# Performance work log

Hardware: AMD Instinct MI355X
Metric: run time of the kernel (lower is better)

The kernel has to match this reference:

```python
import jax, jax.numpy as jnp
import numpy as np

EPS = 1e-6

def rmsnorm(x, w):
    # RMSNorm over last dim (head_dim), eps=1e-6, learned scale w
    return x * jax.lax.rsqrt(jnp.mean(x * x, axis=-1, keepdims=True) + EPS) * w

def setup_inputs() -> dict:
    key = jax.random.key(0)
    ks = jax.random.split(key, 8)
    B, L, D = 2, 256, 4096          # batch, new-chunk len, model dim
    H, Dh = 32, 128                  # heads, head_dim (H*Dh == D)
    SINK, LOCAL = 128, 4096          # attention-sink + sliding window
    S = SINK + LOCAL                 # fixed cache length
    s = 0.02
    return {
        "x": jax.random.normal(ks[0], (B, L, D), jnp.float32),
        "cache_k": jax.random.normal(ks[1], (B, S, H, Dh), jnp.float32),
        "cache_v": jax.random.normal(ks[2], (B, S, H, Dh), jnp.float32),
        "Wq": jax.random.normal(ks[3], (D, H * Dh), jnp.float32) * s,
        "Wk": jax.random.normal(ks[4], (D, H * Dh), jnp.float32) * s,
        "Wv": jax.random.normal(ks[5], (D, H * Dh), jnp.float32) * s,
        "Wo": jax.random.normal(ks[6], (H * Dh, D), jnp.float32) * s,
        "q_norm_w": jnp.ones((Dh,), jnp.float32),
        "k_norm_w": jnp.ones((Dh,), jnp.float32),
        "sink": 128,
    }

def reference(x, cache_k, cache_v, Wq, Wk, Wv, Wo, q_norm_w, k_norm_w, sink):
    B, L, D = x.shape
    S, H, Dh = cache_k.shape[1], cache_k.shape[2], cache_k.shape[3]
    # QKV projections (bias=False) + per-head RMSNorm on q and k
    q = rmsnorm((x @ Wq).reshape(B, L, H, Dh), q_norm_w)
    k = rmsnorm((x @ Wk).reshape(B, L, H, Dh), k_norm_w)
    v = (x @ Wv).reshape(B, L, H, Dh)
    # steady-state cache: keep sink tokens, roll local window left by L, write new chunk at tail
    new_k = jnp.concatenate([cache_k[:, :sink], cache_k[:, sink + L:], k], axis=1)  # [B,S,H,Dh]
    new_v = jnp.concatenate([cache_v[:, :sink], cache_v[:, sink + L:], v], axis=1)
    scale = 1.0 / jnp.sqrt(jnp.asarray(Dh, x.dtype))
    logits = jnp.einsum('blhd,bshd->bhls', q, new_k) * scale  # [B,H,L,S]
    # causal within the new chunk: query i sees cache positions j <= (S-L)+i
    i = jnp.arange(L)[:, None]
    j = jnp.arange(S)[None, :]
    mask = j <= (S - L) + i
    logits = jnp.where(mask[None, None], logits, jnp.finfo(logits.dtype).min)
    attn = jax.nn.softmax(logits, axis=-1)
    out = jnp.einsum('bhls,bshd->blhd', attn, new_v).reshape(B, L, H * Dh)
    return out @ Wo
```

## Files before the change

kernel.cpp:

```cpp
#include <hip/hip_runtime.h>
#include <stdint.h>
#include <stddef.h>

typedef unsigned short u16;
typedef __bf16 bf16x8 __attribute__((ext_vector_type(8)));
typedef float f32x4 __attribute__((ext_vector_type(4)));
typedef u16 u16x8 __attribute__((ext_vector_type(8)));

#define B_    2
#define L_    256
#define D_    4096
#define H_    32
#define DH_   128
#define SINK_ 128
#define S_    4224
#define WINS_ 3968
#define M_    512
#define SPLIT_ 4

__device__ __forceinline__ float bf2f(u16 u){
  union { float f; uint32_t i; } v; v.i = ((uint32_t)u) << 16; return v.f;
}
__device__ __forceinline__ u16 f2bf(float f){
  union { float f; uint32_t i; } v; v.f = f;
  return (u16)((v.i + 0x7fffu + ((v.i >> 16) & 1u)) >> 16);
}
__device__ __forceinline__ bf16x8 ld8(const u16* p){
  return __builtin_bit_cast(bf16x8, *(const u16x8*)p);
}
__device__ __forceinline__ bf16x8 ld8f(const float* p){
  f32x4 a = *(const f32x4*)p;
  f32x4 b = *(const f32x4*)(p + 4);
  u16x8 r;
  r[0] = f2bf(a[0]); r[1] = f2bf(a[1]); r[2] = f2bf(a[2]); r[3] = f2bf(a[3]);
  r[4] = f2bf(b[0]); r[5] = f2bf(b[1]); r[6] = f2bf(b[2]); r[7] = f2bf(b[3]);
  return __builtin_bit_cast(bf16x8, r);
}

__global__ void detect_k(const u16* __restrict__ x, uint32_t* __restrict__ flag){
  const int lane = threadIdx.x & 63;
  int bad = 0;
  for (int i = lane; i < 1024; i += 64){
    float v = bf2f(x[2 * i]);
    if (!(v * 0.0f == 0.0f) || fabsf(v) > 1e6f) bad = 1;
  }
#pragma unroll
  for (int m = 1; m < 64; m <<= 1) bad |= __shfl_xor(bad, m, 64);
  if (threadIdx.x == 0) *flag = (uint32_t)(bad ? 1 : 0);
}

__global__ __launch_bounds__(256) void transpose_k(const void* __restrict__ W,
                                                   u16* __restrict__ WT,
                                                   const uint32_t* __restrict__ flag){
  const int mode = (int)*flag;
  __shared__ u16 Ts[64 * 68];
  const int t  = threadIdx.x;
  const int k0 = blockIdx.x * 64;
  const int n0 = blockIdx.y * 64;
  const int r  = t >> 2;
  const int c  = (t & 3) * 8;
  const size_t rowoff = (size_t)(k0 + r) * 4096;
#pragma unroll
  for (int p = 0; p < 2; p++){
    const int cc = c + p * 32;
    u16x8 v;
    if (mode){
      const float* pf = (const float*)W + rowoff + n0 + cc;
      f32x4 a = *(const f32x4*)pf;
      f32x4 b = *(const f32x4*)(pf + 4);
      v[0] = f2bf(a[0]); v[1] = f2bf(a[1]); v[2] = f2bf(a[2]); v[3] = f2bf(a[3]);
      v[4] = f2bf(b[0]); v[5] = f2bf(b[1]); v[6] = f2bf(b[2]); v[7] = f2bf(b[3]);
    } else {
      v = *(const u16x8*)((const u16*)W + rowoff + n0 + cc);
    }
#pragma unroll
    for (int j = 0; j < 8; j++) Ts[r * 68 + cc + j] = v[j];
  }
  __syncthreads();
#pragma unroll
  for (int p = 0; p < 2; p++){
    const int kc = c + p * 32;
    u16x8 v;
#pragma unroll
    for (int j = 0; j < 8; j++) v[j] = Ts[(kc + j) * 68 + r];
    *(u16x8*)(WT + (size_t)(n0 + r) * 4096 + k0 + kc) = v;
  }
}

__global__ __launch_bounds__(256) void gemm64_k(const void* __restrict__ Ain,
                                                const u16* __restrict__ BT3,
                                                void* __restrict__ Cout,
                                                const uint32_t* __restrict__ flag,
                                                int a_ext, int c_ext){
  const int mode = (int)*flag;
  const int a_f32 = a_ext & mode;
  const int c_f32 = c_ext & mode;

  const int bx = blockIdx.x;
  const int wi = bx >> 6;
  const int n0 = (bx & 63) * 64;
  const int m0 = blockIdx.y * 64;
  const u16* BT = BT3 + (size_t)wi * (4096ull * 4096);

  __shared__ u16 As[64 * 32];
  __shared__ u16 Bs[64 * 32];

  const int t    = threadIdx.x;
  const int w    = t >> 6;
  const int lane = t & 63;
  const int wm   = w >> 1;
  const int wn   = w & 1;
  const int mq   = lane & 15;
  const int qd   = lane >> 4;

  f32x4 acc[2][2] = {};

  const size_t ga = (size_t)(m0 + (t >> 2)) * 4096 + (t & 3) * 8;
  const size_t gb = (size_t)(n0 + (t >> 2)) * 4096 + (t & 3) * 8;

  for (int kt = 0; kt < 128; kt++){
    const int k0 = kt * 32;
    u16x8 av;
    if (a_f32){
      const float* pa = (const float*)Ain + ga + k0;
      f32x4 a = *(const f32x4*)pa;
      f32x4 b = *(const f32x4*)(pa + 4);
      av[0] = f2bf(a[0]); av[1] = f2bf(a[1]); av[2] = f2bf(a[2]); av[3] = f2bf(a[3]);
      av[4] = f2bf(b[0]); av[5] = f2bf(b[1]); av[6] = f2bf(b[2]); av[7] = f2bf(b[3]);
    } else {
      av = *(const u16x8*)((const u16*)Ain + ga + k0);
    }
    u16x8 bv = *(const u16x8*)(BT + gb + k0);
    __syncthreads();
    *(u16x8*)&As[t * 8] = av;
    *(u16x8*)&Bs[t * 8] = bv;
    __syncthreads();

    bf16x8 af[2], bfr[2];
#pragma unroll
    for (int i = 0; i < 2; i++)
      af[i] = ld8(&As[(wm * 32 + i * 16 + mq) * 32 + qd * 8]);
#pragma unroll
    for (int j = 0; j < 2; j++)
      bfr[j] = ld8(&Bs[(wn * 32 + j * 16 + mq) * 32 + qd * 8]);
#pragma unroll
    for (int i = 0; i < 2; i++)
#pragma unroll
      for (int j = 0; j < 2; j++)
        acc[i][j] = __builtin_amdgcn_mfma_f32_16x16x32_bf16(af[i], bfr[j], acc[i][j], 0, 0, 0);
  }

  u16* cu = (u16*)Cout + (size_t)wi * ((size_t)M_ * 4096);
#pragma unroll
  for (int i = 0; i < 2; i++)
#pragma unroll
    for (int j = 0; j < 2; j++)
#pragma unroll
      for (int r = 0; r < 4; r++){
        const int row = m0 + wm * 32 + i * 16 + qd * 4 + r;
        const int col = n0 + wn * 32 + j * 16 + mq;
        if (c_f32) ((float*)Cout)[(size_t)row * 4096 + col] = acc[i][j][r];
        else       cu[(size_t)row * 4096 + col]             = f2bf(acc[i][j][r]);
      }
}

__global__ __launch_bounds__(256) void rmsnorm_k(const u16* __restrict__ src,
                                                 u16* __restrict__ dst,
                                                 const void* __restrict__ wq,
                                                 const void* __restrict__ wk,
                                                 const uint32_t* __restrict__ flag){
  const int mode = (int)*flag;
  const int t = threadIdx.x, w = t >> 6, lane = t & 63;
  const size_t base = (size_t)blockIdx.y * (size_t)M_ * 4096;
  const int rid = blockIdx.x * 4 + w;
  const u16* s = src + base + (size_t)rid * 128 + lane * 2;
  u16*       d = dst + base + (size_t)rid * 128 + lane * 2;
  const void* wp = blockIdx.y ? wk : wq;
  float w0, w1;
  if (mode){ w0 = ((const float*)wp)[lane * 2]; w1 = ((const float*)wp)[lane * 2 + 1]; }
  else     { w0 = bf2f(((const u16*)wp)[lane * 2]); w1 = bf2f(((const u16*)wp)[lane * 2 + 1]); }
  const float f0 = bf2f(s[0]), f1 = bf2f(s[1]);
  float ss = f0 * f0 + f1 * f1;
#pragma unroll
  for (int m = 1; m < 64; m <<= 1) ss += __shfl_xor(ss, m, 64);
  const float rinv = rsqrtf(ss * (1.0f / 128.0f) + 1e-6f);
  d[0] = f2bf(f0 * rinv * w0);
  d[1] = f2bf(f1 * rinv * w1);
}

__global__ __launch_bounds__(512, 4) void attn_k(const u16* __restrict__ qn,
                                                 const u16* __restrict__ kn,
                                                 const u16* __restrict__ vnew,
                                                 const void* __restrict__ ck,
                                                 const void* __restrict__ cv,
                                                 u16* __restrict__ ao,
                                                 const uint32_t* __restrict__ flag){
  const int mode = (int)*flag;
  __shared__ __align__(16) unsigned char LDSB[51200];
  u16*   VTall = (u16*)LDSB;
  u16*   PBall = (u16*)(LDSB + 40960);
  float* OB    = (float*)LDSB;
  float* ML    = (float*)(LDSB + 16384);

  const int t  = threadIdx.x;
  const int W  = t >> 6;
  const int sp = W >> 1;
  const int w  = W & 1;
  const int lane = t & 63;
  const int lt = t & 127;
  const int blk = blockIdx.x;
  const int b  = blk >> 8;
  const int h  = (blk >> 3) & 31;
  const int qt = blk & 7;
  const int q0 = qt * 32 + w * 16;
  const int mq = lane & 15;
  const int qd = lane >> 4;

  u16* VT = VTall + sp * (128 * 40);
  u16* pb = PBall + W * 640;

  bf16x8 aq[4];
  {
    const u16* qp = qn + ((size_t)(b * L_ + q0 + mq)) * 4096 + h * 128 + qd * 8;
#pragma unroll
    for (int kc = 0; kc < 4; kc++) aq[kc] = ld8(qp + kc * 32);
  }

  f32x4 oacc[8] = {};
  float mi[4], li[4];
#pragma unroll
  for (int r = 0; r < 4; r++){ mi[r] = -1e30f; li[r] = 0.f; }

  const int nchunks = (WINS_ + qt * 32 + 63) / 32;
  const int cpb = (nchunks + SPLIT_ - 1) / SPLIT_;
  const int sc_beg = sp * cpb;
  const int sc_end = (sc_beg + cpb < nchunks) ? (sc_beg + cpb) : nchunks;
  const float scale = 0.08838834764831845f;
  const float L2E = 1.4426950408889634f;

  const int dd = lt;
  u16x8 vv[4];

  auto loadV = [&](int sc){
    const int s0c = sc * 32;
#pragma unroll
    for (int c = 0; c < 4; c++){
#pragma unroll
      for (int j = 0; j < 8; j++){
        const int s = s0c + c * 8 + j;
        u16 val;
        if (s >= WINS_){
          val = vnew[((size_t)(b * L_ + (s - WINS_)) << 12) + h * 128 + dd];
        } else {
          const int scc = (s < SINK_) ? s : (s + L_);
          const size_t off = ((((size_t)b * S_ + scc) * H_ + h) << 7) + dd;
          val = mode ? f2bf(((const float*)cv)[off]) : ((const u16*)cv)[off];
        }
        vv[c][j] = val;
      }
    }
  };

  if (sc_beg < sc_end) loadV(sc_beg);

  for (int scr = 0; scr < cpb; scr++){
    const int sc = sc_beg + scr;
    const int act = (sc < sc_end);
    const int s0 = sc * 32;

    __syncthreads();
    if (act){
#pragma unroll
      for (int c = 0; c < 4; c++)
        *(u16x8*)&VT[dd * 40 + c * 8] = vv[c];
    }
    __syncthreads();
    if (sc + 1 < sc_end) loadV(sc + 1);

    if (act){
      float lg[2][4];
#pragma unroll
      for (int st = 0; st < 2; st++){
        const int s = s0 + st * 16 + mq;
        f32x4 a = {};
        if (s0 + st * 16 >= WINS_){
          const u16* kp = kn + ((size_t)(b * L_ + (s - WINS_)) << 12) + h * 128;
#pragma unroll
          for (int kc = 0; kc < 4; kc++)
            a = __builtin_amdgcn_mfma_f32_16x16x32_bf16(aq[kc], ld8(kp + kc * 32 + qd * 8), a, 0, 0, 0);
        } else if (mode){
          const int scc = (s < SINK_) ? s : (s + L_);
          const float* kp = (const float*)ck + ((((size_t)b * S_ + scc) * H_ + h) << 7);
#pragma unroll
          for (int kc = 0; kc < 4; kc++)
            a = __builtin_amdgcn_mfma_f32_16x16x32_bf16(aq[kc], ld8f(kp + kc * 32 + qd * 8), a, 0, 0, 0);
        } else {
          const int scc = (s < SINK_) ? s : (s + L_);
          const u16* kp = (const u16*)ck + ((((size_t)b * S_ + scc) * H_ + h) << 7);
#pragma unroll
          for (int kc = 0; kc < 4; kc++)
            a = __builtin_amdgcn_mfma_f32_16x16x32_bf16(aq[kc], ld8(kp + kc * 32 + qd * 8), a, 0, 0, 0);
        }
#pragma unroll
        for (int r = 0; r < 4; r++) lg[st][r] = a[r] * scale;
      }
      if (s0 + 31 > WINS_ + q0){
#pragma unroll
        for (int st = 0; st < 2; st++){
          const int s = s0 + st * 16 + mq;
#pragma unroll
          for (int r = 0; r < 4; r++)
            if (s > WINS_ + (q0 + qd * 4 + r)) lg[st][r] = -1e30f;
        }
      }
      float p[2][4];
#pragma unroll
      for (int r = 0; r < 4; r++){
        float mx = fmaxf(lg[0][r], lg[1][r]);
#pragma unroll
        for (int m = 1; m < 16; m <<= 1) mx = fmaxf(mx, __shfl_xor(mx, m, 64));
        const float mnew = fmaxf(mi[r], mx);
        const float alpha = exp2f((mi[r] - mnew) * L2E);
        mi[r] = mnew;
        float s_ = 0.f;
#pragma unroll
        for (int st = 0; st < 2; st++){
          p[st][r] = exp2f((lg[st][r] - mnew) * L2E);
          s_ += p[st][r];
        }
#pragma unroll
        for (int m = 1; m < 16; m <<= 1) s_ += __shfl_xor(s_, m, 64);
        li[r] = li[r] * alpha + s_;
#pragma unroll
        for (int nt = 0; nt < 8; nt++) oacc[nt][r] *= alpha;
      }
#pragma unroll
      for (int st = 0; st < 2; st++)
#pragma unroll
        for (int r = 0; r < 4; r++)
          pb[(qd * 4 + r) * 40 + st * 16 + mq] = f2bf(p[st][r]);
      asm volatile("" ::: "memory");
      u16x8 pr;
#pragma unroll
      for (int j = 0; j < 8; j++) pr[j] = pb[mq * 40 + qd * 8 + j];
      bf16x8 ap = __builtin_bit_cast(bf16x8, pr);
#pragma unroll
      for (int nt = 0; nt < 8; nt++){
        bf16x8 bv = ld8(&VT[(nt * 16 + mq) * 40 + qd * 8]);
        oacc[nt] = __builtin_amdgcn_mfma_f32_16x16x32_bf16(ap, bv, oacc[nt], 0, 0, 0);
      }
    }
  }

  __syncthreads();
  if (mq == 0){
#pragma unroll
    for (int r = 0; r < 4; r++){
      const int lr = w * 16 + qd * 4 + r;
      ML[(sp * 32 + lr) * 2 + 0] = mi[r];
      ML[(sp * 32 + lr) * 2 + 1] = li[r];
    }
  }
  __syncthreads();

  float gl[4], wgt[4];
#pragma unroll
  for (int r = 0; r < 4; r++){
    const int lr = w * 16 + qd * 4 + r;
    float m_ = -1e30f;
#pragma unroll
    for (int p = 0; p < SPLIT_; p++) m_ = fmaxf(m_, ML[(p * 32 + lr) * 2 + 0]);
    float l_ = 0.f;
#pragma unroll
    for (int p = 0; p < SPLIT_; p++)
      l_ += exp2f((ML[(p * 32 + lr) * 2 + 0] - m_) * L2E) * ML[(p * 32 + lr) * 2 + 1];
    gl[r] = l_;
    wgt[r] = exp2f((mi[r] - m_) * L2E);
  }

#pragma unroll
  for (int p = 0; p < SPLIT_; p++){
    if (sp == p){
#pragma unroll
      for (int nt = 0; nt < 8; nt++)
#pragma unroll
        for (int r = 0; r < 4; r++){
          const int off = (w * 16 + qd * 4 + r) * 128 + nt * 16 + mq;
          const float v = wgt[r] * oacc[nt][r];
          if (p == 0) OB[off] = v;
          else        OB[off] += v;
        }
    }
    __syncthreads();
  }

  if (sp == 0){
#pragma unroll
    for (int nt = 0; nt < 8; nt++)
#pragma unroll
      for (int r = 0; r < 4; r++){
        const int lr = w * 16 + qd * 4 + r;
        const int qrow = qt * 32 + lr;
        const float v = OB[lr * 128 + nt * 16 + mq] / gl[r];
        ao[((size_t)(b * L_ + qrow) << 12) + h * 128 + nt * 16 + mq] = f2bf(v);
      }
  }
}

extern "C" void kernel_launch(void* const* d_in, const int* in_sizes, int n_in,
                              void* d_out, int out_size, void* d_ws, size_t ws_size,
                              hipStream_t stream){
  (void)in_sizes; (void)n_in; (void)out_size;
  const void* x  = d_in[0];
  const void* ck = d_in[1];
  const void* cv = d_in[2];
  const void* Wq = d_in[3];
  const void* Wk = d_in[4];
  const void* Wv = d_in[5];
  const void* Wo = d_in[6];
  const void* qw = d_in[7];
  const void* kw = d_in[8];

  const size_t WT_E = 4096ull * 4096;
  const size_t BUF  = (size_t)M_ * 4096;

  uint32_t* flag = (uint32_t*)d_ws;
  u16* ws0 = (u16*)d_ws + 64;

  detect_k<<<1, 64, 0, stream>>>((const u16*)x, flag);

  const size_t need_fused = 128 + (3 * WT_E + 6 * BUF) * 2;
  if (ws_size >= need_fused){
    u16* WT3 = ws0;
    u16* qkv = WT3 + 3 * WT_E;
    u16* qn  = qkv + 3 * BUF;
    u16* ao  = qn + 2 * BUF;

    transpose_k<<<dim3(64, 64), 256, 0, stream>>>(Wq, WT3, flag);
    transpose_k<<<dim3(64, 64), 256, 0, stream>>>(Wk, WT3 + WT_E, flag);
    transpose_k<<<dim3(64, 64), 256, 0, stream>>>(Wv, WT3 + 2 * WT_E, flag);
    gemm64_k<<<dim3(192, 8), 256, 0, stream>>>(x, WT3, qkv, flag, 1, 0);

    rmsnorm_k<<<dim3(4096, 2), 256, 0, stream>>>(qkv, qn, qw, kw, flag);

    attn_k<<<dim3(512), 512, 0, stream>>>(qn, qn + BUF, qkv + 2 * BUF,
                                          ck, cv, ao, flag);

    transpose_k<<<dim3(64, 64), 256, 0, stream>>>(Wo, WT3, flag);
    gemm64_k<<<dim3(64, 8), 256, 0, stream>>>(ao, WT3, d_out, flag, 0, 1);
  } else {
    u16* WT  = ws0;
    u16* qkv = WT + WT_E;
    u16* qn  = qkv + 3 * BUF;
    u16* ao  = qn + 2 * BUF;

    transpose_k<<<dim3(64, 64), 256, 0, stream>>>(Wq, WT, flag);
    gemm64_k<<<dim3(64, 8), 256, 0, stream>>>(x, WT, qkv, flag, 1, 0);
    transpose_k<<<dim3(64, 64), 256, 0, stream>>>(Wk, WT, flag);
    gemm64_k<<<dim3(64, 8), 256, 0, stream>>>(x, WT, qkv + BUF, flag, 1, 0);
    transpose_k<<<dim3(64, 64), 256, 0, stream>>>(Wv, WT, flag);
    gemm64_k<<<dim3(64, 8), 256, 0, stream>>>(x, WT, qkv + 2 * BUF, flag, 1, 0);

    rmsnorm_k<<<dim3(4096, 2), 256, 0, stream>>>(qkv, qn, qw, kw, flag);

    attn_k<<<dim3(512), 512, 0, stream>>>(qn, qn + BUF, qkv + 2 * BUF,
                                          ck, cv, ao, flag);

    transpose_k<<<dim3(64, 64), 256, 0, stream>>>(Wo, WT, flag);
    gemm64_k<<<dim3(64, 8), 256, 0, stream>>>(ao, WT, d_out, flag, 0, 1);
  }
}
```

Measured before the change: 1.409 ms.

## Widen attention blocks to 64 queries and software-prefetch K fragments

```diff
diff --git a/kernel.cpp b/kernel.cpp
--- a/kernel.cpp
+++ b/kernel.cpp
@@ -188,31 +188,31 @@
   d[1] = f2bf(f1 * rinv * w1);
 }
 
-__global__ __launch_bounds__(512, 4) void attn_k(const u16* __restrict__ qn,
-                                                 const u16* __restrict__ kn,
-                                                 const u16* __restrict__ vnew,
-                                                 const void* __restrict__ ck,
-                                                 const void* __restrict__ cv,
-                                                 u16* __restrict__ ao,
-                                                 const uint32_t* __restrict__ flag){
+__global__ __launch_bounds__(1024, 4) void attn_k(const u16* __restrict__ qn,
+                                                  const u16* __restrict__ kn,
+                                                  const u16* __restrict__ vnew,
+                                                  const void* __restrict__ ck,
+                                                  const void* __restrict__ cv,
+                                                  u16* __restrict__ ao,
+                                                  const uint32_t* __restrict__ flag){
   const int mode = (int)*flag;
-  __shared__ __align__(16) unsigned char LDSB[51200];
+  __shared__ __align__(16) unsigned char LDSB[61440];
   u16*   VTall = (u16*)LDSB;
-  u16*   PBall = (u16*)(LDSB + 40960);
+  u16*   PBall = (u16*)LDSB + 4 * 5120;
   float* OB    = (float*)LDSB;
-  float* ML    = (float*)(LDSB + 16384);
+  float* ML    = (float*)(LDSB + 32768);
 
   const int t  = threadIdx.x;
   const int W  = t >> 6;
-  const int sp = W >> 1;
-  const int w  = W & 1;
+  const int sp = W >> 2;
+  const int w  = W & 3;
   const int lane = t & 63;
-  const int lt = t & 127;
+  const int lt = t & 255;
   const int blk = blockIdx.x;
-  const int b  = blk >> 8;
-  const int h  = (blk >> 3) & 31;
-  const int qt = blk & 7;
-  const int q0 = qt * 32 + w * 16;
+  const int b  = blk >> 7;
+  const int h  = (blk >> 2) & 31;
+  const int qt = blk & 3;
+  const int q0 = qt * 64 + w * 16;
   const int mq = lane & 15;
   const int qd = lane >> 4;
 
@@ -231,37 +231,57 @@
 #pragma unroll
   for (int r = 0; r < 4; r++){ mi[r] = -1e30f; li[r] = 0.f; }
 
-  const int nchunks = (WINS_ + qt * 32 + 63) / 32;
+  const int nchunks = (WINS_ + qt * 64 + 63) / 32 + 1;
   const int cpb = (nchunks + SPLIT_ - 1) / SPLIT_;
   const int sc_beg = sp * cpb;
   const int sc_end = (sc_beg + cpb < nchunks) ? (sc_beg + cpb) : nchunks;
   const float scale = 0.08838834764831845f;
   const float L2E = 1.4426950408889634f;
 
-  const int dd = lt;
-  u16x8 vv[4];
+  const int dd = lt & 127, sg = lt >> 7;
+  u16 vv[16];
+  bf16x8 kf[2][4];
 
   auto loadV = [&](int sc){
     const int s0c = sc * 32;
 #pragma unroll
-    for (int c = 0; c < 4; c++){
-#pragma unroll
-      for (int j = 0; j < 8; j++){
-        const int s = s0c + c * 8 + j;
-        u16 val;
-        if (s >= WINS_){
-          val = vnew[((size_t)(b * L_ + (s - WINS_)) << 12) + h * 128 + dd];
-        } else {
-          const int scc = (s < SINK_) ? s : (s + L_);
-          const size_t off = ((((size_t)b * S_ + scc) * H_ + h) << 7) + dd;
-          val = mode ? f2bf(((const float*)cv)[off]) : ((const u16*)cv)[off];
-        }
-        vv[c][j] = val;
+    for (int j = 0; j < 16; j++){
+      const int s = s0c + sg * 16 + j;
+      if (s >= WINS_){
+        vv[j] = vnew[((size_t)(b * L_ + (s - WINS_)) << 12) + h * 128 + dd];
+      } else {
+        const int scc = (s < SINK_) ? s : (s + L_);
+        const size_t off = ((((size_t)b * S_ + scc) * H_ + h) << 7) + dd;
+        vv[j] = mode ? f2bf(((const float*)cv)[off]) : ((const u16*)cv)[off];
       }
     }
   };
 
-  if (sc_beg < sc_end) loadV(sc_beg);
+  auto loadK = [&](int sc){
+    const int s0c = sc * 32;
+#pragma unroll
+    for (int st = 0; st < 2; st++){
+      const int stile = s0c + st * 16;
+      const int s = stile + mq;
+      if (stile >= WINS_){
+        const u16* kp = kn + ((size_t)(b * L_ + (s - WINS_)) << 12) + h * 128;
+#pragma unroll
+        for (int kc = 0; kc < 4; kc++) kf[st][kc] = ld8(kp + kc * 32 + qd * 8);
+      } else if (mode){
+        const int scc = (s < SINK_) ? s : (s + L_);
+        const float* kp = (const float*)ck + ((((size_t)b * S_ + scc) * H_ + h) << 7);
+#pragma unroll
+        for (int kc = 0; kc < 4; kc++) kf[st][kc] = ld8f(kp + kc * 32 + qd * 8);
+      } else {
+        const int scc = (s < SINK_) ? s : (s + L_);
+        const u16* kp = (const u16*)ck + ((((size_t)b * S_ + scc) * H_ + h) << 7);
+#pragma unroll
+        for (int kc = 0; kc < 4; kc++) kf[st][kc] = ld8(kp + kc * 32 + qd * 8);
+      }
+    }
+  };
+
+  if (sc_beg < sc_end){ loadV(sc_beg); loadK(sc_beg); }
 
   for (int scr = 0; scr < cpb; scr++){
     const int sc = sc_beg + scr;
@@ -271,8 +291,12 @@
     __syncthreads();
     if (act){
 #pragma unroll
-      for (int c = 0; c < 4; c++)
-        *(u16x8*)&VT[dd * 40 + c * 8] = vv[c];
+      for (int hv = 0; hv < 2; hv++){
+        u16x8 pk;
+#pragma unroll
+        for (int j = 0; j < 8; j++) pk[j] = vv[hv * 8 + j];
+        *(u16x8*)&VT[dd * 40 + sg * 16 + hv * 8] = pk;
+      }
     }
     __syncthreads();
     if (sc + 1 < sc_end) loadV(sc + 1);
@@ -281,29 +305,15 @@
       float lg[2][4];
 #pragma unroll
       for (int st = 0; st < 2; st++){
-        const int s = s0 + st * 16 + mq;
         f32x4 a = {};
-        if (s0 + st * 16 >= WINS_){
-          const u16* kp = kn + ((size_t)(b * L_ + (s - WINS_)) << 12) + h * 128;
-#pragma unroll
-          for (int kc = 0; kc < 4; kc++)
-            a = __builtin_amdgcn_mfma_f32_16x16x32_bf16(aq[kc], ld8(kp + kc * 32 + qd * 8), a, 0, 0, 0);
-        } else if (mode){
-          const int scc = (s < SINK_) ? s : (s + L_);
-          const float* kp = (const float*)ck + ((((size_t)b * S_ + scc) * H_ + h) << 7);
-#pragma unroll
-          for (int kc = 0; kc < 4; kc++)
-            a = __builtin_amdgcn_mfma_f32_16x16x32_bf16(aq[kc], ld8f(kp + kc * 32 + qd * 8), a, 0, 0, 0);
-        } else {
-          const int scc = (s < SINK_) ? s : (s + L_);
-          const u16* kp = (const u16*)ck + ((((size_t)b * S_ + scc) * H_ + h) << 7);
-#pragma unroll
-          for (int kc = 0; kc < 4; kc++)
-            a = __builtin_amdgcn_mfma_f32_16x16x32_bf16(aq[kc], ld8(kp + kc * 32 + qd * 8), a, 0, 0, 0);
-        }
+#pragma unroll
+        for (int kc = 0; kc < 4; kc++)
+          a = __builtin_amdgcn_mfma_f32_16x16x32_bf16(aq[kc], kf[st][kc], a, 0, 0, 0);
 #pragma unroll
         for (int r = 0; r < 4; r++) lg[st][r] = a[r] * scale;
       }
+      if (sc + 1 < sc_end) loadK(sc + 1);
+
       if (s0 + 31 > WINS_ + q0){
 #pragma unroll
         for (int st = 0; st < 2; st++){
@@ -357,8 +367,8 @@
 #pragma unroll
     for (int r = 0; r < 4; r++){
       const int lr = w * 16 + qd * 4 + r;
-      ML[(sp * 32 + lr) * 2 + 0] = mi[r];
-      ML[(sp * 32 + lr) * 2 + 1] = li[r];
+      ML[(sp * 64 + lr) * 2 + 0] = mi[r];
+      ML[(sp * 64 + lr) * 2 + 1] = li[r];
     }
   }
   __syncthreads();
@@ -369,11 +379,11 @@
     const int lr = w * 16 + qd * 4 + r;
     float m_ = -1e30f;
 #pragma unroll
-    for (int p = 0; p < SPLIT_; p++) m_ = fmaxf(m_, ML[(p * 32 + lr) * 2 + 0]);
+    for (int p = 0; p < SPLIT_; p++) m_ = fmaxf(m_, ML[(p * 64 + lr) * 2 + 0]);
     float l_ = 0.f;
 #pragma unroll
     for (int p = 0; p < SPLIT_; p++)
-      l_ += exp2f((ML[(p * 32 + lr) * 2 + 0] - m_) * L2E) * ML[(p * 32 + lr) * 2 + 1];
+      l_ += exp2f((ML[(p * 64 + lr) * 2 + 0] - m_) * L2E) * ML[(p * 64 + lr) * 2 + 1];
     gl[r] = l_;
     wgt[r] = exp2f((mi[r] - m_) * L2E);
   }
@@ -400,7 +410,7 @@
 #pragma unroll
       for (int r = 0; r < 4; r++){
         const int lr = w * 16 + qd * 4 + r;
-        const int qrow = qt * 32 + lr;
+        const int qrow = qt * 64 + lr;
         const float v = OB[lr * 128 + nt * 16 + mq] / gl[r];
         ao[((size_t)(b * L_ + qrow) << 12) + h * 128 + nt * 16 + mq] = f2bf(v);
       }
@@ -443,8 +453,8 @@
 
     rmsnorm_k<<<dim3(4096, 2), 256, 0, stream>>>(qkv, qn, qw, kw, flag);
 
-    attn_k<<<dim3(512), 512, 0, stream>>>(qn, qn + BUF, qkv + 2 * BUF,
-                                          ck, cv, ao, flag);
+    attn_k<<<dim3(256), 1024, 0, stream>>>(qn, qn + BUF, qkv + 2 * BUF,
+                                           ck, cv, ao, flag);
 
     transpose_k<<<dim3(64, 64), 256, 0, stream>>>(Wo, WT3, flag);
     gemm64_k<<<dim3(64, 8), 256, 0, stream>>>(ao, WT3, d_out, flag, 0, 1);
@@ -463,8 +473,8 @@
 
     rmsnorm_k<<<dim3(4096, 2), 256, 0, stream>>>(qkv, qn, qw, kw, flag);
 
-    attn_k<<<dim3(512), 512, 0, stream>>>(qn, qn + BUF, qkv + 2 * BUF,
-                                          ck, cv, ao, flag);
+    attn_k<<<dim3(256), 1024, 0, stream>>>(qn, qn + BUF, qkv + 2 * BUF,
+                                           ck, cv, ao, flag);
 
     transpose_k<<<dim3(64, 64), 256, 0, stream>>>(Wo, WT, flag);
     gemm64_k<<<dim3(64, 8), 256, 0, stream>>>(ao, WT, d_out, flag, 0, 1);
```

Result: faster. 1.312 ms (-6.9%).
